# Optimization experiments

Measured on AMD Instinct MI355X. Metric: run time of the kernel, lower is better.

Reference implementation:

```python
import jax, jax.numpy as jnp
import numpy as np

N_NODES = 100000
N_EDGES = 1000000
IN_DIM = 32
HID_DIM = 64
NUM_REL = 2
NUM_CLASSES = 2


def setup_inputs() -> dict:
    key = jax.random.key(0)
    ks = jax.random.split(key, 12)
    x = jax.random.normal(ks[0], (N_NODES, IN_DIM), dtype=jnp.float32)
    edge_index = jax.random.randint(ks[1], (2, N_EDGES), 0, N_NODES, dtype=jnp.int32)
    edge_attr = jax.random.randint(ks[2], (N_EDGES, 2), 0, NUM_REL, dtype=jnp.int32)
    s1 = 1.0 / np.sqrt(IN_DIM)
    s2 = 1.0 / np.sqrt(HID_DIM)
    W1 = jax.random.normal(ks[3], (NUM_REL, IN_DIM, HID_DIM), dtype=jnp.float32) * s1
    root1 = jax.random.normal(ks[4], (IN_DIM, HID_DIM), dtype=jnp.float32) * s1
    b1 = jnp.zeros((HID_DIM,), dtype=jnp.float32)
    W2 = jax.random.normal(ks[5], (NUM_REL, HID_DIM, HID_DIM), dtype=jnp.float32) * s2
    root2 = jax.random.normal(ks[6], (HID_DIM, HID_DIM), dtype=jnp.float32) * s2
    b2 = jnp.zeros((HID_DIM,), dtype=jnp.float32)
    Wc = jax.random.normal(ks[7], (HID_DIM, NUM_CLASSES), dtype=jnp.float32) * s2
    bc = jnp.zeros((NUM_CLASSES,), dtype=jnp.float32)
    return {"x": x, "edge_index": edge_index, "edge_attr": edge_attr,
            "W1": W1, "root1": root1, "b1": b1,
            "W2": W2, "root2": root2, "b2": b2,
            "Wc": Wc, "bc": bc}


def _rgcn_conv(x, src, dst, edge_type, W, root, b):
    # PyG RGCNConv (aggr='mean'): out = x @ root + b + sum_r mean_agg_r(x_j) @ W_r
    n = x.shape[0]
    xs = x[src]  # [E, F] gather, shared across relations
    out = x @ root + b
    for r in range(W.shape[0]):
        m = (edge_type == r).astype(x.dtype)  # [E]
        s = jax.ops.segment_sum(xs * m[:, None], dst, num_segments=n)  # [N, F]
        cnt = jax.ops.segment_sum(m, dst, num_segments=n)  # [N]
        h = s / jnp.maximum(cnt, 1.0)[:, None]
        out = out + h @ W[r]
    return out


def reference(x, edge_index, edge_attr, W1, root1, b1, W2, root2, b2, Wc, bc):
    edge_type = edge_attr[:, -1].astype(jnp.int32)
    src, dst = edge_index[0], edge_index[1]
    h = jax.nn.relu(_rgcn_conv(x, src, dst, edge_type, W1, root1, b1))
    # dropout(p=0.2) is identity in eval mode
    h = jax.nn.relu(_rgcn_conv(h, src, dst, edge_type, W2, root2, b2))
    return h @ Wc + bc
```

## Files before the change

kernel.cpp:

```cpp
#include <hip/hip_runtime.h>

#define N_NODES 100000
#define N_EDGES 1000000
#define IN_DIM 32
#define HID_DIM 64
#define N2 (2 * N_NODES)
#define NRANGE 8
#define RNODES (N_NODES / NRANGE)
#define ECHUNK 2048


__global__ __launch_bounds__(256) void k_rd(
    const int* __restrict__ ei, const int* __restrict__ ea,
    int* __restrict__ rd)
{
    int e = blockIdx.x * 256 + threadIdx.x;
    if (e >= N_EDGES) return;
    rd[e] = (ei[N_EDGES + e] << 1) | ea[2 * e + 1];
}


__device__ __forceinline__ unsigned short f2bf(float f) {
    unsigned u = __float_as_uint(f);
    return (unsigned short)((u + 0x7FFFu + ((u >> 16) & 1u)) >> 16);
}

#define ACC4(acc, v, wa, wb, wc_, wd) \
    acc = fmaf((v).x, wa, acc);       \
    acc = fmaf((v).y, wb, acc);       \
    acc = fmaf((v).z, wc_, acc);      \
    acc = fmaf((v).w, wd, acc);

#define MACC4(A, v, m)                \
    A.x = fmaf((v).x, m, A.x);        \
    A.y = fmaf((v).y, m, A.y);        \
    A.z = fmaf((v).z, m, A.z);        \
    A.w = fmaf((v).w, m, A.w);

#define BUNPACK(v_, u) {                           \
    v_.x = __uint_as_float((u).x << 16);           \
    v_.y = __uint_as_float((u).x & 0xFFFF0000u);   \
    v_.z = __uint_as_float((u).y << 16);           \
    v_.w = __uint_as_float((u).y & 0xFFFF0000u);   \
}

#define BMACC4(A, u, m) { float4 v_; BUNPACK(v_, u) MACC4(A, v_, m) }


__global__ __launch_bounds__(256) void k_count(
    const int* __restrict__ rd, int* __restrict__ deg)
{
    int range = blockIdx.x & (NRANGE - 1);
    int chunk = blockIdx.x >> 3;
    int lo = range * RNODES;
    int e0 = chunk * ECHUNK;
    int e1 = min(e0 + ECHUNK, N_EDGES);
    for (int e = e0 + threadIdx.x; e < e1; e += 256) {
        int v = rd[e];
        int dst = v >> 1;
        if ((unsigned)(dst - lo) < (unsigned)RNODES)
            atomicAdd(&deg[(v & 1) * N_NODES + dst], 1);
    }
}

__global__ __launch_bounds__(256) void k_scan_local(
    const int* __restrict__ deg, int* __restrict__ offs, int* __restrict__ bsum)
{
    int t = threadIdx.x;
    int i = blockIdx.x * 256 + t;
    int v = (i < N2) ? deg[i] : 0;
    int lane = t & 63, w = t >> 6;
    int s = v;
#pragma unroll
    for (int off = 1; off < 64; off <<= 1) {
        int u = __shfl_up(s, off);
        if (lane >= off) s += u;
    }
    __shared__ int wsum[4];
    if (lane == 63) wsum[w] = s;
    __syncthreads();
    int add = 0;
    for (int ww = 0; ww < w; ++ww) add += wsum[ww];
    s += add;
    if (i < N2) offs[i] = s - v;
    if (t == 255) bsum[blockIdx.x] = s;
}

__global__ __launch_bounds__(64) void k_scan_blocks(int* __restrict__ bsum, int nblk)
{
    int lane = threadIdx.x;
    int carry = 0;
    for (int base = 0; base < nblk; base += 64) {
        int i = base + lane;
        int v = (i < nblk) ? bsum[i] : 0;
        int s = v;
#pragma unroll
        for (int off = 1; off < 64; off <<= 1) {
            int u = __shfl_up(s, off);
            if (lane >= off) s += u;
        }
        if (i < nblk) bsum[i] = carry + s - v;
        carry += __shfl(s, 63);
    }
}

__global__ __launch_bounds__(256) void k_scan_add(
    const int* __restrict__ offs, const int* __restrict__ bsum,
    const int* __restrict__ deg,
    int* __restrict__ cursor, int2* __restrict__ od)
{
    int i = blockIdx.x * 256 + threadIdx.x;
    if (i >= N2) return;
    int o = offs[i] + bsum[i >> 8];
    cursor[i] = o;
    od[i] = make_int2(o, deg[i]);
}

__global__ __launch_bounds__(256) void k_fill(
    const int* __restrict__ rd, const int* __restrict__ ei,
    int* __restrict__ cursor, int* __restrict__ elist)
{
    int range = blockIdx.x & (NRANGE - 1);
    int chunk = blockIdx.x >> 3;
    int lo = range * RNODES;
    int e0 = chunk * ECHUNK;
    int e1 = min(e0 + ECHUNK, N_EDGES);
    for (int e = e0 + threadIdx.x; e < e1; e += 256) {
        int v = rd[e];
        int dst = v >> 1;
        if ((unsigned)(dst - lo) < (unsigned)RNODES) {
            int src = ei[e];
            int pos = atomicAdd(&cursor[(v & 1) * N_NODES + dst], 1);
            elist[pos] = src;
        }
    }
}


__global__ __launch_bounds__(512, 4) void k_gemm1(
    const float* __restrict__ x,
    const float* __restrict__ root1,
    const float* __restrict__ W1,
    const float* __restrict__ b1,
    unsigned short* __restrict__ Rb,
    unsigned short* __restrict__ Y)
{
    __shared__ float wR[IN_DIM * HID_DIM];
    __shared__ float w0[IN_DIM * HID_DIM];
    __shared__ float w1s[IN_DIM * HID_DIM];
    int tid = threadIdx.x;
    for (int i = tid; i < IN_DIM * HID_DIM; i += 512) {
        wR[i]  = root1[i];
        w0[i]  = W1[i];
        w1s[i] = W1[IN_DIM * HID_DIM + i];
    }
    __syncthreads();

    int j  = tid & 63;
    int n0 = __builtin_amdgcn_readfirstlane(blockIdx.x * 32 + ((tid >> 6) << 2));
    const float* px = x + (size_t)n0 * IN_DIM;

    float accR0 = 0, accR1 = 0, accR2 = 0, accR3 = 0;
    float acc00 = 0, acc01 = 0, acc02 = 0, acc03 = 0;
    float acc10 = 0, acc11 = 0, acc12 = 0, acc13 = 0;

#pragma unroll 1
    for (int kk = 0; kk < IN_DIM / 4; ++kk) {
        int kbase = kk * 4;
        float4 xv0 = *(const float4*)(px + 0 * IN_DIM + kbase);
        float4 xv1 = *(const float4*)(px + 1 * IN_DIM + kbase);
        float4 xv2 = *(const float4*)(px + 2 * IN_DIM + kbase);
        float4 xv3 = *(const float4*)(px + 3 * IN_DIM + kbase);
        int wb_i = kbase * 64 + j;
        float wRa = wR[wb_i], wRb = wR[wb_i + 64], wRc = wR[wb_i + 128], wRd = wR[wb_i + 192];
        float w0a = w0[wb_i], w0b = w0[wb_i + 64], w0c = w0[wb_i + 128], w0d = w0[wb_i + 192];
        float w1a = w1s[wb_i], w1b = w1s[wb_i + 64], w1c = w1s[wb_i + 128], w1d = w1s[wb_i + 192];

        ACC4(accR0, xv0, wRa, wRb, wRc, wRd)
        ACC4(accR1, xv1, wRa, wRb, wRc, wRd)
        ACC4(accR2, xv2, wRa, wRb, wRc, wRd)
        ACC4(accR3, xv3, wRa, wRb, wRc, wRd)
        ACC4(acc00, xv0, w0a, w0b, w0c, w0d)
        ACC4(acc01, xv1, w0a, w0b, w0c, w0d)
        ACC4(acc02, xv2, w0a, w0b, w0c, w0d)
        ACC4(acc03, xv3, w0a, w0b, w0c, w0d)
        ACC4(acc10, xv0, w1a, w1b, w1c, w1d)
        ACC4(acc11, xv1, w1a, w1b, w1c, w1d)
        ACC4(acc12, xv2, w1a, w1b, w1c, w1d)
        ACC4(acc13, xv3, w1a, w1b, w1c, w1d)
    }

    float bj = b1[j];
    Rb[(size_t)(n0 + 0) * HID_DIM + j] = f2bf(accR0 + bj);
    Rb[(size_t)(n0 + 1) * HID_DIM + j] = f2bf(accR1 + bj);
    Rb[(size_t)(n0 + 2) * HID_DIM + j] = f2bf(accR2 + bj);
    Rb[(size_t)(n0 + 3) * HID_DIM + j] = f2bf(accR3 + bj);
    unsigned short* Y0 = Y;
    unsigned short* Y1 = Y + (size_t)N_NODES * HID_DIM;
    Y0[(size_t)(n0 + 0) * HID_DIM + j] = f2bf(acc00);
    Y0[(size_t)(n0 + 1) * HID_DIM + j] = f2bf(acc01);
    Y0[(size_t)(n0 + 2) * HID_DIM + j] = f2bf(acc02);
    Y0[(size_t)(n0 + 3) * HID_DIM + j] = f2bf(acc03);
    Y1[(size_t)(n0 + 0) * HID_DIM + j] = f2bf(acc10);
    Y1[(size_t)(n0 + 1) * HID_DIM + j] = f2bf(acc11);
    Y1[(size_t)(n0 + 2) * HID_DIM + j] = f2bf(acc12);
    Y1[(size_t)(n0 + 3) * HID_DIM + j] = f2bf(acc13);
}

__global__ __launch_bounds__(512, 4) void k_gemm2(
    const unsigned short* __restrict__ h1b,
    const float* __restrict__ root2,
    const float* __restrict__ W2,
    const float* __restrict__ b2,
    unsigned short* __restrict__ Rb,
    unsigned short* __restrict__ Y)
{
    __shared__ float wR[HID_DIM * HID_DIM];
    __shared__ float w0[HID_DIM * HID_DIM];
    __shared__ float w1s[HID_DIM * HID_DIM];
    int tid = threadIdx.x;
    for (int i = tid; i < HID_DIM * HID_DIM; i += 512) {
        wR[i]  = root2[i];
        w0[i]  = W2[i];
        w1s[i] = W2[HID_DIM * HID_DIM + i];
    }
    __syncthreads();

    int j  = tid & 63;
    int n0 = __builtin_amdgcn_readfirstlane(blockIdx.x * 32 + ((tid >> 6) << 2));
    const unsigned short* pb = h1b + (size_t)n0 * HID_DIM;

    float accR0 = 0, accR1 = 0, accR2 = 0, accR3 = 0;
    float acc00 = 0, acc01 = 0, acc02 = 0, acc03 = 0;
    float acc10 = 0, acc11 = 0, acc12 = 0, acc13 = 0;

#pragma unroll 1
    for (int kk = 0; kk < HID_DIM / 4; ++kk) {
        int kbase = kk * 4;
        uint2 u0 = *(const uint2*)(pb + 0 * HID_DIM + kbase);
        uint2 u1 = *(const uint2*)(pb + 1 * HID_DIM + kbase);
        uint2 u2 = *(const uint2*)(pb + 2 * HID_DIM + kbase);
        uint2 u3 = *(const uint2*)(pb + 3 * HID_DIM + kbase);
        float4 xv0, xv1, xv2, xv3;
        BUNPACK(xv0, u0) BUNPACK(xv1, u1) BUNPACK(xv2, u2) BUNPACK(xv3, u3)
        int wb_i = kbase * 64 + j;
        float wRa = wR[wb_i], wRb = wR[wb_i + 64], wRc = wR[wb_i + 128], wRd = wR[wb_i + 192];
        float w0a = w0[wb_i], w0b = w0[wb_i + 64], w0c = w0[wb_i + 128], w0d = w0[wb_i + 192];
        float w1a = w1s[wb_i], w1b = w1s[wb_i + 64], w1c = w1s[wb_i + 128], w1d = w1s[wb_i + 192];

        ACC4(accR0, xv0, wRa, wRb, wRc, wRd)
        ACC4(accR1, xv1, wRa, wRb, wRc, wRd)
        ACC4(accR2, xv2, wRa, wRb, wRc, wRd)
        ACC4(accR3, xv3, wRa, wRb, wRc, wRd)
        ACC4(acc00, xv0, w0a, w0b, w0c, w0d)
        ACC4(acc01, xv1, w0a, w0b, w0c, w0d)
        ACC4(acc02, xv2, w0a, w0b, w0c, w0d)
        ACC4(acc03, xv3, w0a, w0b, w0c, w0d)
        ACC4(acc10, xv0, w1a, w1b, w1c, w1d)
        ACC4(acc11, xv1, w1a, w1b, w1c, w1d)
        ACC4(acc12, xv2, w1a, w1b, w1c, w1d)
        ACC4(acc13, xv3, w1a, w1b, w1c, w1d)
    }

    float bj = b2[j];
    Rb[(size_t)(n0 + 0) * HID_DIM + j] = f2bf(accR0 + bj);
    Rb[(size_t)(n0 + 1) * HID_DIM + j] = f2bf(accR1 + bj);
    Rb[(size_t)(n0 + 2) * HID_DIM + j] = f2bf(accR2 + bj);
    Rb[(size_t)(n0 + 3) * HID_DIM + j] = f2bf(accR3 + bj);
    unsigned short* Y0 = Y;
    unsigned short* Y1 = Y + (size_t)N_NODES * HID_DIM;
    Y0[(size_t)(n0 + 0) * HID_DIM + j] = f2bf(acc00);
    Y0[(size_t)(n0 + 1) * HID_DIM + j] = f2bf(acc01);
    Y0[(size_t)(n0 + 2) * HID_DIM + j] = f2bf(acc02);
    Y0[(size_t)(n0 + 3) * HID_DIM + j] = f2bf(acc03);
    Y1[(size_t)(n0 + 0) * HID_DIM + j] = f2bf(acc10);
    Y1[(size_t)(n0 + 1) * HID_DIM + j] = f2bf(acc11);
    Y1[(size_t)(n0 + 2) * HID_DIM + j] = f2bf(acc12);
    Y1[(size_t)(n0 + 3) * HID_DIM + j] = f2bf(acc13);
}


__global__ __launch_bounds__(512, 8) void k_gather1(
    const unsigned short* __restrict__ Y,
    const unsigned short* __restrict__ Rb,
    const int2* __restrict__ od,
    const int* __restrict__ elist,
    unsigned short* __restrict__ h1b)
{
    int tid = threadIdx.x;
    int lane = tid & 63;
    int wv   = __builtin_amdgcn_readfirstlane(tid >> 6);
    int n0   = __builtin_amdgcn_readfirstlane(blockIdx.x * 32 + wv * 4);

    int sub  = lane >> 4;
    int node = n0 + sub;
    int q    = lane & 15;
    int base = lane & 48;

    const unsigned short* Y0 = Y;
    const unsigned short* Y1 = Y + (size_t)N_NODES * HID_DIM;

    int2 o0 = od[node];
    int2 o1 = od[N_NODES + node];
    int d0 = o0.y, d1 = o1.y;
    int er0 = (q < d0) ? elist[o0.x + q] : 0;
    int er1 = (q < d1) ? elist[o1.x + q] : 0;

    int dm = max(d0, d1);
    dm = max(dm, __shfl_xor(dm, 16));
    dm = max(dm, __shfl_xor(dm, 32));
    int kend = min(dm, 16);

    float4 A0 = make_float4(0.f, 0.f, 0.f, 0.f);
    float4 A1 = make_float4(0.f, 0.f, 0.f, 0.f);
    for (int k = 0; k < kend; ++k) {
        int i0 = __shfl(er0, base + k);
        int i1 = __shfl(er1, base + k);
        uint2 u0 = *(const uint2*)(Y0 + (size_t)i0 * HID_DIM + q * 4);
        uint2 u1 = *(const uint2*)(Y1 + (size_t)i1 * HID_DIM + q * 4);
        float m0 = (k < d0) ? 1.0f : 0.0f;
        float m1 = (k < d1) ? 1.0f : 0.0f;
        BMACC4(A0, u0, m0)
        BMACC4(A1, u1, m1)
    }
    if (dm > 16) {
        for (int k = 16; k < dm; ++k) {
            int i0 = 0, i1 = 0;
            if (k < d0) i0 = elist[o0.x + k];
            if (k < d1) i1 = elist[o1.x + k];
            uint2 u0 = *(const uint2*)(Y0 + (size_t)i0 * HID_DIM + q * 4);
            uint2 u1 = *(const uint2*)(Y1 + (size_t)i1 * HID_DIM + q * 4);
            float m0 = (k < d0) ? 1.0f : 0.0f;
            float m1 = (k < d1) ? 1.0f : 0.0f;
            BMACC4(A0, u0, m0)
            BMACC4(A1, u1, m1)
        }
    }
    float i0v = 1.0f / fmaxf((float)d0, 1.0f);
    float i1v = 1.0f / fmaxf((float)d1, 1.0f);
    uint2 ru = *(const uint2*)(Rb + (size_t)node * HID_DIM + q * 4);
    float4 Rq; BUNPACK(Rq, ru)
    ushort4 o;
    o.x = f2bf(fmaxf(Rq.x + A0.x * i0v + A1.x * i1v, 0.0f));
    o.y = f2bf(fmaxf(Rq.y + A0.y * i0v + A1.y * i1v, 0.0f));
    o.z = f2bf(fmaxf(Rq.z + A0.z * i0v + A1.z * i1v, 0.0f));
    o.w = f2bf(fmaxf(Rq.w + A0.w * i0v + A1.w * i1v, 0.0f));
    *(ushort4*)(h1b + (size_t)node * HID_DIM + q * 4) = o;
}

__global__ __launch_bounds__(512, 8) void k_gather2(
    const unsigned short* __restrict__ Y,
    const unsigned short* __restrict__ Rb,
    const int2* __restrict__ od,
    const int* __restrict__ elist,
    const float* __restrict__ Wc,
    const float* __restrict__ bc,
    float* __restrict__ out)
{
    int tid = threadIdx.x;
    int lane = tid & 63;
    int wv   = __builtin_amdgcn_readfirstlane(tid >> 6);
    int n0   = __builtin_amdgcn_readfirstlane(blockIdx.x * 32 + wv * 4);

    int sub  = lane >> 4;
    int node = n0 + sub;
    int q    = lane & 15;
    int base = lane & 48;

    const unsigned short* Y0 = Y;
    const unsigned short* Y1 = Y + (size_t)N_NODES * HID_DIM;

    int2 o0 = od[node];
    int2 o1 = od[N_NODES + node];
    int d0 = o0.y, d1 = o1.y;
    int er0 = (q < d0) ? elist[o0.x + q] : 0;
    int er1 = (q < d1) ? elist[o1.x + q] : 0;

    int dm = max(d0, d1);
    dm = max(dm, __shfl_xor(dm, 16));
    dm = max(dm, __shfl_xor(dm, 32));
    int kend = min(dm, 16);

    float4 A0 = make_float4(0.f, 0.f, 0.f, 0.f);
    float4 A1 = make_float4(0.f, 0.f, 0.f, 0.f);
    for (int k = 0; k < kend; ++k) {
        int i0 = __shfl(er0, base + k);
        int i1 = __shfl(er1, base + k);
        uint2 u0 = *(const uint2*)(Y0 + (size_t)i0 * HID_DIM + q * 4);
        uint2 u1 = *(const uint2*)(Y1 + (size_t)i1 * HID_DIM + q * 4);
        float m0 = (k < d0) ? 1.0f : 0.0f;
        float m1 = (k < d1) ? 1.0f : 0.0f;
        BMACC4(A0, u0, m0)
        BMACC4(A1, u1, m1)
    }
    if (dm > 16) {
        for (int k = 16; k < dm; ++k) {
            int i0 = 0, i1 = 0;
            if (k < d0) i0 = elist[o0.x + k];
            if (k < d1) i1 = elist[o1.x + k];
            uint2 u0 = *(const uint2*)(Y0 + (size_t)i0 * HID_DIM + q * 4);
            uint2 u1 = *(const uint2*)(Y1 + (size_t)i1 * HID_DIM + q * 4);
            float m0 = (k < d0) ? 1.0f : 0.0f;
            float m1 = (k < d1) ? 1.0f : 0.0f;
            BMACC4(A0, u0, m0)
            BMACC4(A1, u1, m1)
        }
    }
    float i0v = 1.0f / fmaxf((float)d0, 1.0f);
    float i1v = 1.0f / fmaxf((float)d1, 1.0f);
    uint2 ru = *(const uint2*)(Rb + (size_t)node * HID_DIM + q * 4);
    float4 Rq; BUNPACK(Rq, ru)
    float4 h2;
    h2.x = fmaxf(Rq.x + A0.x * i0v + A1.x * i1v, 0.0f);
    h2.y = fmaxf(Rq.y + A0.y * i0v + A1.y * i1v, 0.0f);
    h2.z = fmaxf(Rq.z + A0.z * i0v + A1.z * i1v, 0.0f);
    h2.w = fmaxf(Rq.w + A0.w * i0v + A1.w * i1v, 0.0f);

    float4 wcA = *(const float4*)(Wc + 8 * q);
    float4 wcB = *(const float4*)(Wc + 8 * q + 4);
    float v0 = h2.x * wcA.x + h2.y * wcA.z + h2.z * wcB.x + h2.w * wcB.z;
    float v1 = h2.x * wcA.y + h2.y * wcA.w + h2.z * wcB.y + h2.w * wcB.w;
#pragma unroll
    for (int off = 1; off <= 8; off <<= 1) {
        v0 += __shfl_xor(v0, off);
        v1 += __shfl_xor(v1, off);
    }
    if (q == 0) {
        out[(size_t)node * 2 + 0] = v0 + bc[0];
        out[(size_t)node * 2 + 1] = v1 + bc[1];
    }
}


extern "C" void kernel_launch(void* const* d_in, const int* in_sizes, int n_in,
                              void* d_out, int out_size, void* d_ws, size_t ws_size,
                              hipStream_t stream) {
    const float* x     = (const float*)d_in[0];
    const int*   ei    = (const int*)d_in[1];
    const int*   ea    = (const int*)d_in[2];
    const float* W1    = (const float*)d_in[3];
    const float* root1 = (const float*)d_in[4];
    const float* b1    = (const float*)d_in[5];
    const float* W2    = (const float*)d_in[6];
    const float* root2 = (const float*)d_in[7];
    const float* b2    = (const float*)d_in[8];
    const float* Wc    = (const float*)d_in[9];
    const float* bc    = (const float*)d_in[10];
    float* out = (float*)d_out;

    char* ws = (char*)d_ws;
    int*   deg    = (int*)(ws);
    int*   offs   = (int*)(ws + 800000);
    int2*  od     = (int2*)(ws + 1600000);
    int*   elist  = (int*)(ws + 3200000);
    int*   cursor = (int*)(ws + 7200000);
    int*   bsum   = (int*)(ws + 8000000);
    int*   rd     = (int*)(ws + 8004096);
    unsigned short* Y   = (unsigned short*)(ws + 12004096);
    unsigned short* Rb  = (unsigned short*)(ws + 37604096);
    unsigned short* h1b = (unsigned short*)(ws + 50404096);

    const int nblk_scan = (N2 + 255) / 256;
    const int grid_e    = (N_EDGES + 255) / 256;
    const int grid_cf   = ((N_EDGES + ECHUNK - 1) / ECHUNK) * NRANGE;
    const int grid_n    = N_NODES / 32;

    hipMemsetAsync(deg, 0, (size_t)N2 * 4, stream);
    k_rd<<<grid_e, 256, 0, stream>>>(ei, ea, rd);
    k_count<<<grid_cf, 256, 0, stream>>>(rd, deg);
    k_scan_local<<<nblk_scan, 256, 0, stream>>>(deg, offs, bsum);
    k_scan_blocks<<<1, 64, 0, stream>>>(bsum, nblk_scan);
    k_scan_add<<<nblk_scan, 256, 0, stream>>>(offs, bsum, deg, cursor, od);
    k_fill<<<grid_cf, 256, 0, stream>>>(rd, ei, cursor, elist);

    k_gemm1<<<grid_n, 512, 0, stream>>>(x, root1, W1, b1, Rb, Y);
    k_gather1<<<grid_n, 512, 0, stream>>>(Y, Rb, od, elist, h1b);

    k_gemm2<<<grid_n, 512, 0, stream>>>(h1b, root2, W2, b2, Rb, Y);
    k_gather2<<<grid_n, 512, 0, stream>>>(Y, Rb, od, elist, Wc, bc, out);
}
```

Before: 230.8 us.

## Replace scalar FMA node GEMMs with bf16 MFMA 16x16x32 kernels

Both per-layer dense transforms (root plus two relation weights) now run on bf16 MFMA instructions instead of scalar FMAs over LDS-staged weights. Two new prep kernels convert x to bf16 and pre-pack the weight matrices into MFMA B-fragment layout, so the GEMM kernels read fragments straight from global memory with no shared memory or barrier. This cuts ALU time and LDS traffic in the GEMM stages, but adds two small launches and rounds x and the weights to bf16, which costs some accuracy.

```diff
diff --git a/kernel.cpp b/kernel.cpp
--- a/kernel.cpp
+++ b/kernel.cpp
@@ -9,6 +9,10 @@
 #define RNODES (N_NODES / NRANGE)
 #define ECHUNK 2048
 
+typedef __attribute__((ext_vector_type(8))) short bf16x8;
+typedef __attribute__((ext_vector_type(4))) float f32x4;
+#define MFMA16x32 __builtin_amdgcn_mfma_f32_16x16x32_bf16
+
 
 __global__ __launch_bounds__(256) void k_rd(
     const int* __restrict__ ei, const int* __restrict__ ea,
@@ -24,12 +28,6 @@
     unsigned u = __float_as_uint(f);
     return (unsigned short)((u + 0x7FFFu + ((u >> 16) & 1u)) >> 16);
 }
-
-#define ACC4(acc, v, wa, wb, wc_, wd) \
-    acc = fmaf((v).x, wa, acc);       \
-    acc = fmaf((v).y, wb, acc);       \
-    acc = fmaf((v).z, wc_, acc);      \
-    acc = fmaf((v).w, wd, acc);
 
 #define MACC4(A, v, m)                \
     A.x = fmaf((v).x, m, A.x);        \
@@ -45,6 +43,43 @@
 }
 
 #define BMACC4(A, u, m) { float4 v_; BUNPACK(v_, u) MACC4(A, v_, m) }
+
+__global__ __launch_bounds__(256) void k_xb(
+    const float* __restrict__ x, unsigned short* __restrict__ xb)
+{
+    int i = blockIdx.x * 256 + threadIdx.x;
+    if (i >= N_NODES * IN_DIM / 4) return;
+    float4 v = ((const float4*)x)[i];
+    ushort4 o;
+    o.x = f2bf(v.x); o.y = f2bf(v.y); o.z = f2bf(v.z); o.w = f2bf(v.w);
+    ((ushort4*)xb)[i] = o;
+}
+
+__global__ __launch_bounds__(256) void k_wpack(
+    const float* __restrict__ root1, const float* __restrict__ W1,
+    const float* __restrict__ root2, const float* __restrict__ W2,
+    unsigned short* __restrict__ wb1, unsigned short* __restrict__ wb2)
+{
+    int idx = blockIdx.x * 256 + threadIdx.x;
+    if (idx < 6144) {
+        int e = idx & 7, lane = (idx >> 3) & 63, fid = idx >> 9;
+        int jt = fid & 3, mat = fid >> 2;
+        int k = (lane >> 4) * 8 + e;
+        int j = jt * 16 + (lane & 15);
+        float v = (mat == 0) ? root1[k * 64 + j]
+                             : W1[(mat - 1) * (IN_DIM * HID_DIM) + k * 64 + j];
+        wb1[idx] = f2bf(v);
+    } else if (idx < 6144 + 12288) {
+        int i2 = idx - 6144;
+        int e = i2 & 7, lane = (i2 >> 3) & 63, fid = i2 >> 9;
+        int jt = fid & 3, ks = (fid >> 2) & 1, mat = fid >> 3;
+        int k = ks * 32 + (lane >> 4) * 8 + e;
+        int j = jt * 16 + (lane & 15);
+        float v = (mat == 0) ? root2[k * 64 + j]
+                             : W2[(mat - 1) * (HID_DIM * HID_DIM) + k * 64 + j];
+        wb2[i2] = f2bf(v);
+    }
+}
 
 
 __global__ __launch_bounds__(256) void k_count(
@@ -137,146 +172,122 @@
 }
 
 
-__global__ __launch_bounds__(512, 4) void k_gemm1(
-    const float* __restrict__ x,
-    const float* __restrict__ root1,
-    const float* __restrict__ W1,
+__global__ __launch_bounds__(512, 8) void k_mgemm1(
+    const unsigned short* __restrict__ xb,
+    const unsigned short* __restrict__ wb1,
     const float* __restrict__ b1,
     unsigned short* __restrict__ Rb,
     unsigned short* __restrict__ Y)
 {
-    __shared__ float wR[IN_DIM * HID_DIM];
-    __shared__ float w0[IN_DIM * HID_DIM];
-    __shared__ float w1s[IN_DIM * HID_DIM];
     int tid = threadIdx.x;
-    for (int i = tid; i < IN_DIM * HID_DIM; i += 512) {
-        wR[i]  = root1[i];
-        w0[i]  = W1[i];
-        w1s[i] = W1[IN_DIM * HID_DIM + i];
-    }
-    __syncthreads();
-
-    int j  = tid & 63;
-    int n0 = __builtin_amdgcn_readfirstlane(blockIdx.x * 32 + ((tid >> 6) << 2));
-    const float* px = x + (size_t)n0 * IN_DIM;
-
-    float accR0 = 0, accR1 = 0, accR2 = 0, accR3 = 0;
-    float acc00 = 0, acc01 = 0, acc02 = 0, acc03 = 0;
-    float acc10 = 0, acc11 = 0, acc12 = 0, acc13 = 0;
-
-#pragma unroll 1
-    for (int kk = 0; kk < IN_DIM / 4; ++kk) {
-        int kbase = kk * 4;
-        float4 xv0 = *(const float4*)(px + 0 * IN_DIM + kbase);
-        float4 xv1 = *(const float4*)(px + 1 * IN_DIM + kbase);
-        float4 xv2 = *(const float4*)(px + 2 * IN_DIM + kbase);
-        float4 xv3 = *(const float4*)(px + 3 * IN_DIM + kbase);
-        int wb_i = kbase * 64 + j;
-        float wRa = wR[wb_i], wRb = wR[wb_i + 64], wRc = wR[wb_i + 128], wRd = wR[wb_i + 192];
-        float w0a = w0[wb_i], w0b = w0[wb_i + 64], w0c = w0[wb_i + 128], w0d = w0[wb_i + 192];
-        float w1a = w1s[wb_i], w1b = w1s[wb_i + 64], w1c = w1s[wb_i + 128], w1d = w1s[wb_i + 192];
-
-        ACC4(accR0, xv0, wRa, wRb, wRc, wRd)
-        ACC4(accR1, xv1, wRa, wRb, wRc, wRd)
-        ACC4(accR2, xv2, wRa, wRb, wRc, wRd)
-        ACC4(accR3, xv3, wRa, wRb, wRc, wRd)
-        ACC4(acc00, xv0, w0a, w0b, w0c, w0d)
-        ACC4(acc01, xv1, w0a, w0b, w0c, w0d)
-        ACC4(acc02, xv2, w0a, w0b, w0c, w0d)
-        ACC4(acc03, xv3, w0a, w0b, w0c, w0d)
-        ACC4(acc10, xv0, w1a, w1b, w1c, w1d)
-        ACC4(acc11, xv1, w1a, w1b, w1c, w1d)
-        ACC4(acc12, xv2, w1a, w1b, w1c, w1d)
-        ACC4(acc13, xv3, w1a, w1b, w1c, w1d)
-    }
-
-    float bj = b1[j];
-    Rb[(size_t)(n0 + 0) * HID_DIM + j] = f2bf(accR0 + bj);
-    Rb[(size_t)(n0 + 1) * HID_DIM + j] = f2bf(accR1 + bj);
-    Rb[(size_t)(n0 + 2) * HID_DIM + j] = f2bf(accR2 + bj);
-    Rb[(size_t)(n0 + 3) * HID_DIM + j] = f2bf(accR3 + bj);
+    int lane = tid & 63;
+    int wv   = tid >> 6;
+    int n0   = blockIdx.x * 128 + wv * 16;
+
+    int srcn = min(n0 + (lane & 15), N_NODES - 1);
+    bf16x8 a = *(const bf16x8*)(xb + (size_t)srcn * IN_DIM + (lane >> 4) * 8);
+
+    f32x4 z = {0.f, 0.f, 0.f, 0.f};
+    f32x4 cR0 = z, cR1 = z, cR2 = z, cR3 = z;
+    f32x4 c00 = z, c01 = z, c02 = z, c03 = z;
+    f32x4 c10 = z, c11 = z, c12 = z, c13 = z;
+
+#define B1FRAG(mat, jt) (*(const bf16x8*)(wb1 + ((mat) * 4 + (jt)) * 512 + lane * 8))
+    cR0 = MFMA16x32(a, B1FRAG(0, 0), cR0, 0, 0, 0);
+    cR1 = MFMA16x32(a, B1FRAG(0, 1), cR1, 0, 0, 0);
+    cR2 = MFMA16x32(a, B1FRAG(0, 2), cR2, 0, 0, 0);
+    cR3 = MFMA16x32(a, B1FRAG(0, 3), cR3, 0, 0, 0);
+    c00 = MFMA16x32(a, B1FRAG(1, 0), c00, 0, 0, 0);
+    c01 = MFMA16x32(a, B1FRAG(1, 1), c01, 0, 0, 0);
+    c02 = MFMA16x32(a, B1FRAG(1, 2), c02, 0, 0, 0);
+    c03 = MFMA16x32(a, B1FRAG(1, 3), c03, 0, 0, 0);
+    c10 = MFMA16x32(a, B1FRAG(2, 0), c10, 0, 0, 0);
+    c11 = MFMA16x32(a, B1FRAG(2, 1), c11, 0, 0, 0);
+    c12 = MFMA16x32(a, B1FRAG(2, 2), c12, 0, 0, 0);
+    c13 = MFMA16x32(a, B1FRAG(2, 3), c13, 0, 0, 0);
+#undef B1FRAG
+
+    if (n0 >= N_NODES) return;
     unsigned short* Y0 = Y;
     unsigned short* Y1 = Y + (size_t)N_NODES * HID_DIM;
-    Y0[(size_t)(n0 + 0) * HID_DIM + j] = f2bf(acc00);
-    Y0[(size_t)(n0 + 1) * HID_DIM + j] = f2bf(acc01);
-    Y0[(size_t)(n0 + 2) * HID_DIM + j] = f2bf(acc02);
-    Y0[(size_t)(n0 + 3) * HID_DIM + j] = f2bf(acc03);
-    Y1[(size_t)(n0 + 0) * HID_DIM + j] = f2bf(acc10);
-    Y1[(size_t)(n0 + 1) * HID_DIM + j] = f2bf(acc11);
-    Y1[(size_t)(n0 + 2) * HID_DIM + j] = f2bf(acc12);
-    Y1[(size_t)(n0 + 3) * HID_DIM + j] = f2bf(acc13);
-}
-
-__global__ __launch_bounds__(512, 4) void k_gemm2(
+    int col   = lane & 15;
+    int rbase = n0 + (lane >> 4) * 4;
+
+#define OUT1(cR, cA, cB, jt)                                          \
+    {                                                                 \
+        int j = (jt) * 16 + col;                                      \
+        float bj = b1[j];                                             \
+        _Pragma("unroll")                                             \
+        for (int r = 0; r < 4; ++r) {                                 \
+            size_t node = (size_t)(rbase + r);                        \
+            Rb[node * HID_DIM + j] = f2bf(cR[r] + bj);                \
+            Y0[node * HID_DIM + j] = f2bf(cA[r]);                     \
+            Y1[node * HID_DIM + j] = f2bf(cB[r]);                     \
+        }                                                             \
+    }
+    OUT1(cR0, c00, c10, 0)
+    OUT1(cR1, c01, c11, 1)
+    OUT1(cR2, c02, c12, 2)
+    OUT1(cR3, c03, c13, 3)
+#undef OUT1
+}
+
+__global__ __launch_bounds__(512, 8) void k_mgemm2(
     const unsigned short* __restrict__ h1b,
-    const float* __restrict__ root2,
-    const float* __restrict__ W2,
+    const unsigned short* __restrict__ wb2,
     const float* __restrict__ b2,
     unsigned short* __restrict__ Rb,
     unsigned short* __restrict__ Y)
 {
-    __shared__ float wR[HID_DIM * HID_DIM];
-    __shared__ float w0[HID_DIM * HID_DIM];
-    __shared__ float w1s[HID_DIM * HID_DIM];
     int tid = threadIdx.x;
-    for (int i = tid; i < HID_DIM * HID_DIM; i += 512) {
-        wR[i]  = root2[i];
-        w0[i]  = W2[i];
-        w1s[i] = W2[HID_DIM * HID_DIM + i];
-    }
-    __syncthreads();
-
-    int j  = tid & 63;
-    int n0 = __builtin_amdgcn_readfirstlane(blockIdx.x * 32 + ((tid >> 6) << 2));
-    const unsigned short* pb = h1b + (size_t)n0 * HID_DIM;
-
-    float accR0 = 0, accR1 = 0, accR2 = 0, accR3 = 0;
-    float acc00 = 0, acc01 = 0, acc02 = 0, acc03 = 0;
-    float acc10 = 0, acc11 = 0, acc12 = 0, acc13 = 0;
-
-#pragma unroll 1
-    for (int kk = 0; kk < HID_DIM / 4; ++kk) {
-        int kbase = kk * 4;
-        uint2 u0 = *(const uint2*)(pb + 0 * HID_DIM + kbase);
-        uint2 u1 = *(const uint2*)(pb + 1 * HID_DIM + kbase);
-        uint2 u2 = *(const uint2*)(pb + 2 * HID_DIM + kbase);
-        uint2 u3 = *(const uint2*)(pb + 3 * HID_DIM + kbase);
-        float4 xv0, xv1, xv2, xv3;
-        BUNPACK(xv0, u0) BUNPACK(xv1, u1) BUNPACK(xv2, u2) BUNPACK(xv3, u3)
-        int wb_i = kbase * 64 + j;
-        float wRa = wR[wb_i], wRb = wR[wb_i + 64], wRc = wR[wb_i + 128], wRd = wR[wb_i + 192];
-        float w0a = w0[wb_i], w0b = w0[wb_i + 64], w0c = w0[wb_i + 128], w0d = w0[wb_i + 192];
-        float w1a = w1s[wb_i], w1b = w1s[wb_i + 64], w1c = w1s[wb_i + 128], w1d = w1s[wb_i + 192];
-
-        ACC4(accR0, xv0, wRa, wRb, wRc, wRd)
-        ACC4(accR1, xv1, wRa, wRb, wRc, wRd)
-        ACC4(accR2, xv2, wRa, wRb, wRc, wRd)
-        ACC4(accR3, xv3, wRa, wRb, wRc, wRd)
-        ACC4(acc00, xv0, w0a, w0b, w0c, w0d)
-        ACC4(acc01, xv1, w0a, w0b, w0c, w0d)
-        ACC4(acc02, xv2, w0a, w0b, w0c, w0d)
-        ACC4(acc03, xv3, w0a, w0b, w0c, w0d)
-        ACC4(acc10, xv0, w1a, w1b, w1c, w1d)
-        ACC4(acc11, xv1, w1a, w1b, w1c, w1d)
-        ACC4(acc12, xv2, w1a, w1b, w1c, w1d)
-        ACC4(acc13, xv3, w1a, w1b, w1c, w1d)
-    }
-
-    float bj = b2[j];
-    Rb[(size_t)(n0 + 0) * HID_DIM + j] = f2bf(accR0 + bj);
-    Rb[(size_t)(n0 + 1) * HID_DIM + j] = f2bf(accR1 + bj);
-    Rb[(size_t)(n0 + 2) * HID_DIM + j] = f2bf(accR2 + bj);
-    Rb[(size_t)(n0 + 3) * HID_DIM + j] = f2bf(accR3 + bj);
+    int lane = tid & 63;
+    int wv   = tid >> 6;
+    int n0   = blockIdx.x * 128 + wv * 16;
+
+    int srcn = min(n0 + (lane & 15), N_NODES - 1);
+    const unsigned short* pa = h1b + (size_t)srcn * HID_DIM + (lane >> 4) * 8;
+    bf16x8 a0 = *(const bf16x8*)(pa);
+    bf16x8 a1 = *(const bf16x8*)(pa + 32);
+
+    f32x4 z = {0.f, 0.f, 0.f, 0.f};
+    f32x4 cR0 = z, cR1 = z, cR2 = z, cR3 = z;
+    f32x4 c00 = z, c01 = z, c02 = z, c03 = z;
+    f32x4 c10 = z, c11 = z, c12 = z, c13 = z;
+
+#define B2FRAG(mat, ks, jt) \
+    (*(const bf16x8*)(wb2 + (((mat) * 2 + (ks)) * 4 + (jt)) * 512 + lane * 8))
+#define DO2(cv, mat, jt)                                     \
+    cv = MFMA16x32(a0, B2FRAG(mat, 0, jt), cv, 0, 0, 0);     \
+    cv = MFMA16x32(a1, B2FRAG(mat, 1, jt), cv, 0, 0, 0);
+    DO2(cR0, 0, 0) DO2(cR1, 0, 1) DO2(cR2, 0, 2) DO2(cR3, 0, 3)
+    DO2(c00, 1, 0) DO2(c01, 1, 1) DO2(c02, 1, 2) DO2(c03, 1, 3)
+    DO2(c10, 2, 0) DO2(c11, 2, 1) DO2(c12, 2, 2) DO2(c13, 2, 3)
+#undef DO2
+#undef B2FRAG
+
+    if (n0 >= N_NODES) return;
     unsigned short* Y0 = Y;
     unsigned short* Y1 = Y + (size_t)N_NODES * HID_DIM;
-    Y0[(size_t)(n0 + 0) * HID_DIM + j] = f2bf(acc00);
-    Y0[(size_t)(n0 + 1) * HID_DIM + j] = f2bf(acc01);
-    Y0[(size_t)(n0 + 2) * HID_DIM + j] = f2bf(acc02);
-    Y0[(size_t)(n0 + 3) * HID_DIM + j] = f2bf(acc03);
-    Y1[(size_t)(n0 + 0) * HID_DIM + j] = f2bf(acc10);
-    Y1[(size_t)(n0 + 1) * HID_DIM + j] = f2bf(acc11);
-    Y1[(size_t)(n0 + 2) * HID_DIM + j] = f2bf(acc12);
-    Y1[(size_t)(n0 + 3) * HID_DIM + j] = f2bf(acc13);
+    int col   = lane & 15;
+    int rbase = n0 + (lane >> 4) * 4;
+
+#define OUT2(cR, cA, cB, jt)                                          \
+    {                                                                 \
+        int j = (jt) * 16 + col;                                      \
+        float bj = b2[j];                                             \
+        _Pragma("unroll")                                             \
+        for (int r = 0; r < 4; ++r) {                                 \
+            size_t node = (size_t)(rbase + r);                        \
+            Rb[node * HID_DIM + j] = f2bf(cR[r] + bj);                \
+            Y0[node * HID_DIM + j] = f2bf(cA[r]);                     \
+            Y1[node * HID_DIM + j] = f2bf(cB[r]);                     \
+        }                                                             \
+    }
+    OUT2(cR0, c00, c10, 0)
+    OUT2(cR1, c01, c11, 1)
+    OUT2(cR2, c02, c12, 2)
+    OUT2(cR3, c03, c13, 3)
+#undef OUT2
 }
 
 
@@ -459,23 +470,29 @@
     unsigned short* Y   = (unsigned short*)(ws + 12004096);
     unsigned short* Rb  = (unsigned short*)(ws + 37604096);
     unsigned short* h1b = (unsigned short*)(ws + 50404096);
+    unsigned short* xb  = (unsigned short*)(ws + 63204096);
+    unsigned short* wb1 = (unsigned short*)(ws + 69604096);
+    unsigned short* wb2 = (unsigned short*)(ws + 69616384);
 
     const int nblk_scan = (N2 + 255) / 256;
     const int grid_e    = (N_EDGES + 255) / 256;
     const int grid_cf   = ((N_EDGES + ECHUNK - 1) / ECHUNK) * NRANGE;
+    const int grid_m    = (N_NODES + 127) / 128;
     const int grid_n    = N_NODES / 32;
 
     hipMemsetAsync(deg, 0, (size_t)N2 * 4, stream);
     k_rd<<<grid_e, 256, 0, stream>>>(ei, ea, rd);
+    k_xb<<<(N_NODES * IN_DIM / 4 + 255) / 256, 256, 0, stream>>>(x, xb);
+    k_wpack<<<(6144 + 12288 + 255) / 256, 256, 0, stream>>>(root1, W1, root2, W2, wb1, wb2);
     k_count<<<grid_cf, 256, 0, stream>>>(rd, deg);
     k_scan_local<<<nblk_scan, 256, 0, stream>>>(deg, offs, bsum);
     k_scan_blocks<<<1, 64, 0, stream>>>(bsum, nblk_scan);
     k_scan_add<<<nblk_scan, 256, 0, stream>>>(offs, bsum, deg, cursor, od);
     k_fill<<<grid_cf, 256, 0, stream>>>(rd, ei, cursor, elist);
 
-    k_gemm1<<<grid_n, 512, 0, stream>>>(x, root1, W1, b1, Rb, Y);
+    k_mgemm1<<<grid_m, 512, 0, stream>>>(xb, wb1, b1, Rb, Y);
     k_gather1<<<grid_n, 512, 0, stream>>>(Y, Rb, od, elist, h1b);
 
-    k_gemm2<<<grid_n, 512, 0, stream>>>(h1b, root2, W2, b2, Rb, Y);
+    k_mgemm2<<<grid_m, 512, 0, stream>>>(h1b, wb2, b2, Rb, Y);
     k_gather2<<<grid_n, 512, 0, stream>>>(Y, Rb, od, elist, Wc, bc, out);
 }
```

Measured after the change: 216.2 us. 6.3% less time.
